# Kernel optimization log

Measured on AMD Instinct MI355X. Metric: run time of the kernel, lower is better.

Reference implementation:

```python
import jax, jax.numpy as jnp
import numpy as np
from jax import lax

NUM_CLASSES = 21      # VOC: background (class 0) + 20 fg classes
TOP_K = 200           # max detections kept per (image, class)
CONF_THRESH = 0.01
NMS_THRESH = 0.45
VAR0, VAR1 = 0.1, 0.2 # cfg.VARIANCE
K_PRE = 256           # candidates pre-selected per class before NMS (fixed-shape NMS)


def setup_inputs() -> dict:
    key = jax.random.key(0)
    k1, k2, k3 = jax.random.split(key, 3)
    B, P, C = 32, 8732, NUM_CLASSES
    loc_data = jax.random.normal(k1, (B, P, 4), dtype=jnp.float32)
    conf_data = jax.random.normal(k2, (B, P, C), dtype=jnp.float32)
    u = jax.random.uniform(k3, (P, 4), dtype=jnp.float32)
    # priors in center-offset form: centers in [0,1), w/h in [0.02, 0.32)
    prior_data = jnp.concatenate([u[:, :2], 0.02 + 0.3 * u[:, 2:]], axis=-1)
    return {"loc_data": loc_data, "conf_data": conf_data, "prior_data": prior_data}


def decode(loc, priors):
    # loc, priors: [..., 4]; priors are (cx, cy, w, h)
    centers = priors[..., :2] + loc[..., :2] * VAR0 * priors[..., 2:]
    wh = priors[..., 2:] * jnp.exp(loc[..., 2:] * VAR1)
    xy_min = centers - wh * 0.5
    return jnp.concatenate([xy_min, xy_min + wh], axis=-1)  # (x1,y1,x2,y2)


def pairwise_iou(b):
    # b: [K, 4] corner boxes -> [K, K] IoU
    area = jnp.maximum(b[:, 2] - b[:, 0], 0.0) * jnp.maximum(b[:, 3] - b[:, 1], 0.0)
    lt = jnp.maximum(b[:, None, :2], b[None, :, :2])
    rb = jnp.minimum(b[:, None, 2:], b[None, :, 2:])
    wh = jnp.clip(rb - lt, 0.0)
    inter = wh[..., 0] * wh[..., 1]
    union = area[:, None] + area[None, :] - inter
    return inter / jnp.maximum(union, 1e-9)


def nms_one_class(scores_p, boxes_p4):
    # scores_p: [P], boxes_p4: [P, 4]; fixed-shape NMS -> [TOP_K, 5] (score, x1, y1, x2, y2)
    vals, idx = lax.top_k(scores_p, K_PRE)          # sorted descending
    cand = boxes_p4[idx]                            # [K_PRE, 4]
    valid = vals > CONF_THRESH
    iou = pairwise_iou(cand)                        # [K_PRE, K_PRE]
    ar = jnp.arange(K_PRE)

    def step(keep, i):
        # a kept box suppresses later boxes overlapping it above threshold
        sup = keep[i] & (iou[i] > NMS_THRESH) & (ar > i)
        return keep & (~sup), None

    keep, _ = lax.scan(step, valid, ar)
    kept_scores = jnp.where(keep, vals, 0.0)
    # kept entries are already score-ordered; pull the top TOP_K survivors to the front
    sv, si = lax.top_k(kept_scores, TOP_K)
    out_boxes = jnp.where(sv[:, None] > 0.0, cand[si], 0.0)
    return jnp.concatenate([sv[:, None], out_boxes], axis=-1)  # [TOP_K, 5]


def reference(loc_data, conf_data, prior_data):
    # loc_data: [B, P, 4], conf_data: [B, P, C], prior_data: [P, 4]
    probs = jax.nn.softmax(conf_data, axis=-1)                     # [B, P, C]
    probs_fg = jnp.swapaxes(probs[..., 1:], 1, 2)                  # [B, C-1, P] (skip background)
    boxes = decode(loc_data, prior_data[None, :, :])               # [B, P, 4]
    # vmap over classes, then over batch
    per_class = jax.vmap(nms_one_class, in_axes=(0, None))         # ([C-1,P],[P,4]) -> [C-1,TOP_K,5]
    per_image = jax.vmap(per_class, in_axes=(0, 0))
    return per_image(probs_fg, boxes)                              # [B, C-1, TOP_K, 5]
```

## Files before the change

kernel.cpp:

```cpp
#include <hip/hip_runtime.h>
#include <stdint.h>

typedef unsigned long long ull;
typedef float f4v __attribute__((ext_vector_type(4)));

#define NUM_CLASSES 21
#define NFG 20
#define TOPK 200
#define KPRE 256
#define CONF_TH 0.01f
#define NMS_TH 0.45f
#define VAR0 0.1f
#define VAR1 0.2f
#define NV16 18
#define T16_LO 0x3C23u
#define T16_HI 0x3F81u
#define BSLOT(g) ((g) + ((g) >> 6))

__global__ __launch_bounds__(256) void rownorm16_kernel(
    const float* __restrict__ conf, float2* __restrict__ norm,
    ushort* __restrict__ probs16, int B, int P) {
    __shared__ __align__(16) float buf[256 * NUM_CLASSES];
    __shared__ __align__(16) ushort b16[NFG * 256];
    const int t = threadIdx.x;
    const int nch = (P + 255) >> 8;

    const int id = blockIdx.x;
    int b, chk;
    if ((B & 7) == 0) {
        int r = id & 7, m = id >> 3;
        int q = m / nch;
        b = r + (q << 3);
        chk = m - q * nch;
    } else {
        b = id / nch;
        chk = id - b * nch;
    }
    const int p0 = chk << 8;
    const int cnt = min(256, P - p0);
    const float* src = conf + ((size_t)b * P + p0) * NUM_CLASSES;

    if (cnt == 256) {
        const f4v* s4 = (const f4v*)src;
        f4v* b4 = (f4v*)buf;
#pragma unroll
        for (int k = 0; k < 6; ++k) {
            int i = (k << 8) + t;
            if (i < (256 * NUM_CLASSES) / 4) b4[i] = s4[i];
        }
    } else {
        int n = cnt * NUM_CLASSES;
        for (int i = t; i < n; i += 256) buf[i] = src[i];
    }
    __syncthreads();

    if (t < cnt) {
        const float* row = buf + t * NUM_CLASSES;
        float x[NUM_CLASSES];
        float mx = row[0];
        x[0] = mx;
#pragma unroll
        for (int j = 1; j < NUM_CLASSES; ++j) { x[j] = row[j]; mx = fmaxf(mx, x[j]); }
        float s = 0.f;
#pragma unroll
        for (int j = 0; j < NUM_CLASSES; ++j) { x[j] = expf(x[j] - mx); s += x[j]; }
        norm[(size_t)b * P + p0 + t] = make_float2(mx, s);
#pragma unroll
        for (int c = 1; c < NUM_CLASSES; ++c) {
            float v = x[c] / s;
            b16[(c - 1) * 256 + t] = (ushort)(__float_as_uint(v) >> 16);
        }
    }
    __syncthreads();

    if (cnt == 256) {
        const uint* s32 = (const uint*)b16;
#pragma unroll
        for (int k = 0; k < 10; ++k) {
            int e = (k << 8) + t;
            int c = e >> 7;
            int q = e & 127;
            uint* dstu = (uint*)(probs16 + ((size_t)b * NFG + c) * P + p0);
            dstu[q] = s32[(c << 7) + q];
        }
    } else {
        for (int e = t; e < NFG * cnt; e += 256) {
            int c = e / cnt;
            int f = e - c * cnt;
            probs16[((size_t)b * NFG + c) * P + p0 + f] = b16[c * 256 + f];
        }
    }
}

__global__ __launch_bounds__(KPRE) void nms_topk_kernel(
    const float* __restrict__ conf, const float2* __restrict__ norm,
    const ushort* __restrict__ probs16, const float* __restrict__ loc,
    const float* __restrict__ prior, float* __restrict__ out, int B, int P) {

    __shared__ ull arr[2 * KPRE];
    __shared__ ull arr2[2 * KPRE];
    __shared__ int wsum[2][4];
    __shared__ int s_cnt;
    __shared__ float4 sbox[KPRE + (KPRE >> 6)];
    __shared__ float sarea[KPRE + (KPRE >> 6)];
    __shared__ ull smask[KPRE][5];
    __shared__ ull kept_mask[4];

    const int t = threadIdx.x;
    const int lane = t & 63;
    const int wid = t >> 6;
    const ull lmask_lt = (1ULL << lane) - 1ULL;

    const int g = blockIdx.x;
    int b, c;
    if ((B & 7) == 0) {
        int k = g >> 3;
        b = ((k / NFG) << 3) + (g & 7);
        c = k - (k / NFG) * NFG;
    } else {
        b = g / NFG;
        c = g - (g / NFG) * NFG;
    }
    const int pair = b * NFG + c;
    const int nq = P >> 1;

    unsigned int u2[NV16];
    {
        const uint* sp16 = (const uint*)(probs16 + (size_t)pair * P);
#pragma unroll
        for (int i = 0; i < NV16; ++i) {
            int q = (i << 8) + t;
            u2[i] = (q < nq) ? sp16[q] : 0u;
        }
    }

    {
        unsigned int lo = T16_LO, hi = T16_HI;
        while (hi - lo > 1u) {
            unsigned int mid = lo + ((hi - lo) >> 1);
            int cc = 0;
#pragma unroll
            for (int i = 0; i < NV16; ++i) {
                cc += __popcll(__ballot((u2[i] & 0xFFFFu) >= mid));
                cc += __popcll(__ballot((u2[i] >> 16) >= mid));
            }
            if (cc >= KPRE / 4) lo = mid; else hi = mid;
        }
        if (lane == 0) wsum[0][wid] = (int)lo;
    }
    __syncthreads();
    unsigned int T16 = (unsigned int)min(min(wsum[0][0], wsum[0][1]),
                                         min(wsum[0][2], wsum[0][3]));

    int nval;
    for (int attempt = 0;; ++attempt) {
        if (t == 0) s_cnt = 0;
        __syncthreads();
        int wtot = 0;
#pragma unroll
        for (int i = 0; i < NV16; ++i) {
            wtot += __popcll(__ballot((u2[i] & 0xFFFFu) >= T16));
            wtot += __popcll(__ballot((u2[i] >> 16) >= T16));
        }
        int wbase = 0;
        if (lane == 0) wbase = atomicAdd(&s_cnt, wtot);
        wbase = __shfl(wbase, 0);
        int run = wbase;
#pragma unroll
        for (int i = 0; i < NV16; ++i) {
#pragma unroll
            for (int h = 0; h < 2; ++h) {
                unsigned int bits16 = h ? (u2[i] >> 16) : (u2[i] & 0xFFFFu);
                bool pred = (bits16 >= T16);
                ull bal = __ballot(pred);
                if (pred) {
                    int slot = run + __popcll(bal & lmask_lt);
                    if (slot < 2 * KPRE)
                        arr[slot] = (ull)(unsigned int)((((i << 8) + t) << 1) + h);
                }
                run += __popcll(bal);
            }
        }
        __syncthreads();
        if (s_cnt <= 2 * KPRE || attempt == 1) { nval = min(s_cnt, 2 * KPRE); break; }
        unsigned int lo = T16, hi = T16_HI;
        int it = 0;
        while (hi - lo > 1u) {
            unsigned int mid = lo + ((hi - lo) >> 1);
            int cc = 0;
#pragma unroll
            for (int i = 0; i < NV16; ++i) {
                cc += __popcll(__ballot((u2[i] & 0xFFFFu) >= mid));
                cc += __popcll(__ballot((u2[i] >> 16) >= mid));
            }
            if (lane == 0) wsum[it & 1][wid] = cc;
            __syncthreads();
            int totc = wsum[it & 1][0] + wsum[it & 1][1] + wsum[it & 1][2] + wsum[it & 1][3];
            if (totc >= KPRE) lo = mid; else hi = mid;
            ++it;
        }
        T16 = lo;
    }

    for (int e = t; e < 2 * KPRE; e += KPRE)
        if (e >= nval) arr[e] = (ull)0xFFFFFFFFu;
    __syncthreads();

    const float* cb = conf + (size_t)b * P * NUM_CLASSES + (c + 1);
    const float2* nb = norm + (size_t)b * P;
    ull k0, k1;
    {
        unsigned int pa = (unsigned int)arr[t];
        unsigned int pb2 = (unsigned int)arr[t + KPRE];
        const bool va = (pa < (unsigned int)P);
        const bool vb = (pb2 < (unsigned int)P);
        float xa = 0.f, xb = 0.f;
        float2 ma = make_float2(0.f, 1.f), mb = make_float2(0.f, 1.f);
        if (va) { xa = cb[(size_t)pa * NUM_CLASSES]; ma = nb[pa]; }
        if (vb) { xb = cb[(size_t)pb2 * NUM_CLASSES]; mb = nb[pb2]; }
        if (va) {
            float v = expf(xa - ma.x) / ma.y;
            k0 = ((ull)__float_as_uint(v) << 32) | (unsigned int)(~pa);
        } else k0 = 0ULL;
        if (vb) {
            float v = expf(xb - mb.x) / mb.y;
            k1 = ((ull)__float_as_uint(v) << 32) | (unsigned int)(~pb2);
        } else k1 = 0ULL;
    }
    __syncthreads();

    {
        int lstage = 0;
#pragma unroll
        for (int kk = 2; kk <= 2 * KPRE; kk <<= 1) {
#pragma unroll
            for (int j = kk >> 1; j > 0; j >>= 1) {
                if (j == KPRE) {
                    ull mx = (k0 > k1) ? k0 : k1;
                    ull mn = (k0 > k1) ? k1 : k0;
                    k0 = mx; k1 = mn;
                } else if (j >= 64) {
                    ull* A = (lstage & 1) ? arr : arr2;
                    ++lstage;
                    A[t] = k0; A[t + KPRE] = k1;
                    __syncthreads();
                    ull o0 = A[t ^ j];
                    ull o1 = A[(t + KPRE) ^ j];
                    bool amLow = ((t & j) == 0);
                    bool d0 = ((t & kk) == 0);
                    bool d1 = (((t + KPRE) & kk) == 0);
                    k0 = (d0 == amLow) ? ((k0 > o0) ? k0 : o0) : ((k0 > o0) ? o0 : k0);
                    k1 = (d1 == amLow) ? ((k1 > o1) ? k1 : o1) : ((k1 > o1) ? o1 : k1);
                } else {
                    ull o0 = __shfl_xor(k0, j);
                    ull o1 = __shfl_xor(k1, j);
                    bool amLow = ((t & j) == 0);
                    bool d0 = ((t & kk) == 0);
                    bool d1 = (((t + KPRE) & kk) == 0);
                    k0 = (d0 == amLow) ? ((k0 > o0) ? k0 : o0) : ((k0 > o0) ? o0 : k0);
                    k1 = (d1 == amLow) ? ((k1 > o1) ? k1 : o1) : ((k1 > o1) ? o1 : k1);
                }
            }
        }
    }
    const ull key = k0;

    float v = __uint_as_float((unsigned int)(key >> 32));
    int idx = (int)(~(unsigned int)(key & 0xFFFFFFFFu));
    if (idx < 0 || idx >= P) { idx = 0; v = 0.f; }

    const float4 lv = *(const float4*)(loc + ((size_t)b * P + idx) * 4);
    const float4 pv = *(const float4*)(prior + (size_t)idx * 4);
    float cx = pv.x + (lv.x * VAR0) * pv.z;
    float cy = pv.y + (lv.y * VAR0) * pv.w;
    float w = pv.z * expf(lv.z * VAR1);
    float h = pv.w * expf(lv.w * VAR1);
    float x1 = cx - w * 0.5f;
    float y1 = cy - h * 0.5f;
    float x2 = x1 + w;
    float y2 = y1 + h;
    float myarea = fmaxf(x2 - x1, 0.f) * fmaxf(y2 - y1, 0.f);

    sbox[BSLOT(t)] = make_float4(x1, y1, x2, y2);
    sarea[BSLOT(t)] = myarea;
    __syncthreads();

#pragma unroll
    for (int rep = 0; rep < 3; ++rep) {
        int pid = t + (rep << 8);
        if (pid < 640) {
            int r, w2;
            if (pid < 64)       { r = pid;                w2 = 0; }
            else if (pid < 192) { int q = pid - 64;  r = 64  + (q >> 1); w2 = q & 1; }
            else if (pid < 384) { int q = pid - 192; int q3 = q / 3; r = 128 + q3; w2 = q - 3 * q3; }
            else                { int q = pid - 384; r = 192 + (q >> 2); w2 = q & 3; }
            float4 rb = sbox[BSLOT(r)];
            float ra = sarea[BSLOT(r)];
            ull mm = 0ULL;
            for (int i = 0; i < 64; ++i) {
                int gg = (w2 << 6) + i;
                float4 gb = sbox[BSLOT(gg)];
                float lx = fmaxf(gb.x, rb.x), ly = fmaxf(gb.y, rb.y);
                float rx = fminf(gb.z, rb.z), ry = fminf(gb.w, rb.w);
                float iw = fmaxf(rx - lx, 0.f), ih = fmaxf(ry - ly, 0.f);
                float inter = iw * ih;
                float uni = sarea[BSLOT(gg)] + ra - inter;
                bool s = (inter / fmaxf(uni, 1e-9f)) > NMS_TH;
                mm |= ((ull)(s ? 1u : 0u)) << i;
            }
            smask[r][w2] = mm;
        }
    }
    __syncthreads();

    ull m0 = smask[t][0];
    ull m1 = (wid >= 1) ? smask[t][1] : 0ULL;
    ull m2 = (wid >= 2) ? smask[t][2] : 0ULL;
    ull m3 = (wid >= 3) ? smask[t][3] : 0ULL;
    if (wid == 0) m0 &= lmask_lt;
    else if (wid == 1) m1 &= lmask_lt;
    else if (wid == 2) m2 &= lmask_lt;
    else m3 &= lmask_lt;

    int alive = (v > CONF_TH) ? 1 : 0;
    ull mykept = 0ULL;
#pragma unroll
    for (int w2 = 0; w2 < 4; ++w2) {
        if (wid == w2) {
            if (w2 > 0 && (m0 & kept_mask[0])) alive = 0;
            if (w2 > 1 && (m1 & kept_mask[1])) alive = 0;
            if (w2 > 2 && (m2 & kept_mask[2])) alive = 0;
            ull mw = (w2 == 0) ? m0 : (w2 == 1) ? m1 : (w2 == 2) ? m2 : m3;
            ull validb = __ballot(alive != 0);
            ull todo = __ballot((mw & validb) != 0ULL) & validb;
            ull kept = validb & ~todo;
            while (todo) {
                int i = __builtin_ctzll(todo);
                ull row = __shfl(mw, i);
                if ((row & kept) == 0ULL) kept |= (1ULL << i);
                todo &= (todo - 1ULL);
            }
            mykept = kept;
            alive = (int)((kept >> lane) & 1ULL);
            if (lane == 0) kept_mask[w2] = kept;
        }
        __syncthreads();
    }

    int rank = 0;
#pragma unroll
    for (int w2 = 0; w2 < 4; ++w2)
        if (w2 < wid) rank += __popcll(kept_mask[w2]);
    rank += __popcll(mykept & lmask_lt);
    int total = 0;
#pragma unroll
    for (int w2 = 0; w2 < 4; ++w2) total += __popcll(kept_mask[w2]);

    float* orow = out + (size_t)pair * TOPK * 5;
    if (alive && rank < TOPK) {
        float* o = orow + rank * 5;
        o[0] = v; o[1] = x1; o[2] = y1; o[3] = x2; o[4] = y2;
    }
    if (t < TOPK && t >= total) {
        float* o = orow + t * 5;
        o[0] = 0.f; o[1] = 0.f; o[2] = 0.f; o[3] = 0.f; o[4] = 0.f;
    }
}

extern "C" void kernel_launch(void* const* d_in, const int* in_sizes, int n_in,
                              void* d_out, int out_size, void* d_ws, size_t ws_size,
                              hipStream_t stream) {
    const float* loc = (const float*)d_in[0];
    const float* conf = (const float*)d_in[1];
    const float* prior = (const float*)d_in[2];
    float* out = (float*)d_out;

    int P = in_sizes[2] / 4;
    int B = in_sizes[0] / (4 * P);
    int nch = (P + 255) / 256;

    float2* norm = (float2*)d_ws;
    ushort* probs16 = (ushort*)((char*)d_ws + (size_t)B * P * 8);

    rownorm16_kernel<<<dim3(B * nch), 256, 0, stream>>>(conf, norm, probs16, B, P);
    nms_topk_kernel<<<B * NFG, KPRE, 0, stream>>>(conf, norm, probs16, loc, prior, out, B, P);
}
```

Baseline: 126.8 us.

## Double NMS block to 512 threads, one sort key per thread

Raises the NMS/top-k kernel block size from 256 to 512 threads. Each thread now holds half as many packed fp16 probabilities for the threshold search and one bitonic sort key instead of two. The IoU mask build needs two passes instead of three. The threshold search, compaction and bitonic sort are restructured to match, which cuts per-thread serial work and register pressure but adds more barriers across 8 waves. Threads 256 and up sit idle during the decode and greedy-suppression phases.

```diff
diff --git a/kernel.cpp b/kernel.cpp
--- a/kernel.cpp
+++ b/kernel.cpp
@@ -8,11 +8,12 @@
 #define NFG 20
 #define TOPK 200
 #define KPRE 256
+#define NTHR 512
 #define CONF_TH 0.01f
 #define NMS_TH 0.45f
 #define VAR0 0.1f
 #define VAR1 0.2f
-#define NV16 18
+#define NV9 9
 #define T16_LO 0x3C23u
 #define T16_HI 0x3F81u
 #define BSLOT(g) ((g) + ((g) >> 6))
@@ -92,14 +93,14 @@
     }
 }
 
-__global__ __launch_bounds__(KPRE) void nms_topk_kernel(
+__global__ __launch_bounds__(NTHR) void nms_topk_kernel(
     const float* __restrict__ conf, const float2* __restrict__ norm,
     const ushort* __restrict__ probs16, const float* __restrict__ loc,
     const float* __restrict__ prior, float* __restrict__ out, int B, int P) {
 
     __shared__ ull arr[2 * KPRE];
     __shared__ ull arr2[2 * KPRE];
-    __shared__ int wsum[2][4];
+    __shared__ int wsum[2][8];
     __shared__ int s_cnt;
     __shared__ float4 sbox[KPRE + (KPRE >> 6)];
     __shared__ float sarea[KPRE + (KPRE >> 6)];
@@ -124,12 +125,12 @@
     const int pair = b * NFG + c;
     const int nq = P >> 1;
 
-    unsigned int u2[NV16];
+    unsigned int u2[NV9];
     {
         const uint* sp16 = (const uint*)(probs16 + (size_t)pair * P);
 #pragma unroll
-        for (int i = 0; i < NV16; ++i) {
-            int q = (i << 8) + t;
+        for (int i = 0; i < NV9; ++i) {
+            int q = (i << 9) + t;
             u2[i] = (q < nq) ? sp16[q] : 0u;
         }
     }
@@ -140,17 +141,22 @@
             unsigned int mid = lo + ((hi - lo) >> 1);
             int cc = 0;
 #pragma unroll
-            for (int i = 0; i < NV16; ++i) {
+            for (int i = 0; i < NV9; ++i) {
                 cc += __popcll(__ballot((u2[i] & 0xFFFFu) >= mid));
                 cc += __popcll(__ballot((u2[i] >> 16) >= mid));
             }
-            if (cc >= KPRE / 4) lo = mid; else hi = mid;
+            if (cc >= KPRE / 8) lo = mid; else hi = mid;
         }
         if (lane == 0) wsum[0][wid] = (int)lo;
     }
     __syncthreads();
-    unsigned int T16 = (unsigned int)min(min(wsum[0][0], wsum[0][1]),
-                                         min(wsum[0][2], wsum[0][3]));
+    unsigned int T16;
+    {
+        int m = wsum[0][0];
+#pragma unroll
+        for (int w = 1; w < 8; ++w) m = min(m, wsum[0][w]);
+        T16 = (unsigned int)m;
+    }
 
     int nval;
     for (int attempt = 0;; ++attempt) {
@@ -158,7 +164,7 @@
         __syncthreads();
         int wtot = 0;
 #pragma unroll
-        for (int i = 0; i < NV16; ++i) {
+        for (int i = 0; i < NV9; ++i) {
             wtot += __popcll(__ballot((u2[i] & 0xFFFFu) >= T16));
             wtot += __popcll(__ballot((u2[i] >> 16) >= T16));
         }
@@ -167,7 +173,7 @@
         wbase = __shfl(wbase, 0);
         int run = wbase;
 #pragma unroll
-        for (int i = 0; i < NV16; ++i) {
+        for (int i = 0; i < NV9; ++i) {
 #pragma unroll
             for (int h = 0; h < 2; ++h) {
                 unsigned int bits16 = h ? (u2[i] >> 16) : (u2[i] & 0xFFFFu);
@@ -176,7 +182,7 @@
                 if (pred) {
                     int slot = run + __popcll(bal & lmask_lt);
                     if (slot < 2 * KPRE)
-                        arr[slot] = (ull)(unsigned int)((((i << 8) + t) << 1) + h);
+                        arr[slot] = (ull)(unsigned int)((((i << 9) + t) << 1) + h);
                 }
                 run += __popcll(bal);
             }
@@ -189,43 +195,37 @@
             unsigned int mid = lo + ((hi - lo) >> 1);
             int cc = 0;
 #pragma unroll
-            for (int i = 0; i < NV16; ++i) {
+            for (int i = 0; i < NV9; ++i) {
                 cc += __popcll(__ballot((u2[i] & 0xFFFFu) >= mid));
                 cc += __popcll(__ballot((u2[i] >> 16) >= mid));
             }
             if (lane == 0) wsum[it & 1][wid] = cc;
             __syncthreads();
-            int totc = wsum[it & 1][0] + wsum[it & 1][1] + wsum[it & 1][2] + wsum[it & 1][3];
+            int totc = 0;
+#pragma unroll
+            for (int w = 0; w < 8; ++w) totc += wsum[it & 1][w];
             if (totc >= KPRE) lo = mid; else hi = mid;
             ++it;
         }
         T16 = lo;
     }
 
-    for (int e = t; e < 2 * KPRE; e += KPRE)
-        if (e >= nval) arr[e] = (ull)0xFFFFFFFFu;
+    if (t >= nval) arr[t] = (ull)0xFFFFFFFFu;
     __syncthreads();
 
     const float* cb = conf + (size_t)b * P * NUM_CLASSES + (c + 1);
     const float2* nb = norm + (size_t)b * P;
-    ull k0, k1;
+    ull k0;
     {
         unsigned int pa = (unsigned int)arr[t];
-        unsigned int pb2 = (unsigned int)arr[t + KPRE];
-        const bool va = (pa < (unsigned int)P);
-        const bool vb = (pb2 < (unsigned int)P);
-        float xa = 0.f, xb = 0.f;
-        float2 ma = make_float2(0.f, 1.f), mb = make_float2(0.f, 1.f);
-        if (va) { xa = cb[(size_t)pa * NUM_CLASSES]; ma = nb[pa]; }
-        if (vb) { xb = cb[(size_t)pb2 * NUM_CLASSES]; mb = nb[pb2]; }
-        if (va) {
+        if (pa < (unsigned int)P) {
+            float xa = cb[(size_t)pa * NUM_CLASSES];
+            float2 ma = nb[pa];
             float v = expf(xa - ma.x) / ma.y;
             k0 = ((ull)__float_as_uint(v) << 32) | (unsigned int)(~pa);
-        } else k0 = 0ULL;
-        if (vb) {
-            float v = expf(xb - mb.x) / mb.y;
-            k1 = ((ull)__float_as_uint(v) << 32) | (unsigned int)(~pb2);
-        } else k1 = 0ULL;
+        } else {
+            k0 = 0ULL;
+        }
     }
     __syncthreads();
 
@@ -235,59 +235,49 @@
         for (int kk = 2; kk <= 2 * KPRE; kk <<= 1) {
 #pragma unroll
             for (int j = kk >> 1; j > 0; j >>= 1) {
-                if (j == KPRE) {
-                    ull mx = (k0 > k1) ? k0 : k1;
-                    ull mn = (k0 > k1) ? k1 : k0;
-                    k0 = mx; k1 = mn;
-                } else if (j >= 64) {
+                bool amLow = ((t & j) == 0);
+                bool d0 = ((t & kk) == 0);
+                if (j >= 64) {
                     ull* A = (lstage & 1) ? arr : arr2;
                     ++lstage;
-                    A[t] = k0; A[t + KPRE] = k1;
+                    A[t] = k0;
                     __syncthreads();
                     ull o0 = A[t ^ j];
-                    ull o1 = A[(t + KPRE) ^ j];
-                    bool amLow = ((t & j) == 0);
-                    bool d0 = ((t & kk) == 0);
-                    bool d1 = (((t + KPRE) & kk) == 0);
                     k0 = (d0 == amLow) ? ((k0 > o0) ? k0 : o0) : ((k0 > o0) ? o0 : k0);
-                    k1 = (d1 == amLow) ? ((k1 > o1) ? k1 : o1) : ((k1 > o1) ? o1 : k1);
                 } else {
                     ull o0 = __shfl_xor(k0, j);
-                    ull o1 = __shfl_xor(k1, j);
-                    bool amLow = ((t & j) == 0);
-                    bool d0 = ((t & kk) == 0);
-                    bool d1 = (((t + KPRE) & kk) == 0);
                     k0 = (d0 == amLow) ? ((k0 > o0) ? k0 : o0) : ((k0 > o0) ? o0 : k0);
-                    k1 = (d1 == amLow) ? ((k1 > o1) ? k1 : o1) : ((k1 > o1) ? o1 : k1);
                 }
             }
         }
     }
     const ull key = k0;
 
-    float v = __uint_as_float((unsigned int)(key >> 32));
-    int idx = (int)(~(unsigned int)(key & 0xFFFFFFFFu));
-    if (idx < 0 || idx >= P) { idx = 0; v = 0.f; }
-
-    const float4 lv = *(const float4*)(loc + ((size_t)b * P + idx) * 4);
-    const float4 pv = *(const float4*)(prior + (size_t)idx * 4);
-    float cx = pv.x + (lv.x * VAR0) * pv.z;
-    float cy = pv.y + (lv.y * VAR0) * pv.w;
-    float w = pv.z * expf(lv.z * VAR1);
-    float h = pv.w * expf(lv.w * VAR1);
-    float x1 = cx - w * 0.5f;
-    float y1 = cy - h * 0.5f;
-    float x2 = x1 + w;
-    float y2 = y1 + h;
-    float myarea = fmaxf(x2 - x1, 0.f) * fmaxf(y2 - y1, 0.f);
-
-    sbox[BSLOT(t)] = make_float4(x1, y1, x2, y2);
-    sarea[BSLOT(t)] = myarea;
-    __syncthreads();
-
-#pragma unroll
-    for (int rep = 0; rep < 3; ++rep) {
-        int pid = t + (rep << 8);
+    float v = 0.f, x1 = 0.f, y1 = 0.f, x2 = 0.f, y2 = 0.f;
+    if (t < KPRE) {
+        v = __uint_as_float((unsigned int)(key >> 32));
+        int idx = (int)(~(unsigned int)(key & 0xFFFFFFFFu));
+        if (idx < 0 || idx >= P) { idx = 0; v = 0.f; }
+
+        const float4 lv = *(const float4*)(loc + ((size_t)b * P + idx) * 4);
+        const float4 pv = *(const float4*)(prior + (size_t)idx * 4);
+        float cx = pv.x + (lv.x * VAR0) * pv.z;
+        float cy = pv.y + (lv.y * VAR0) * pv.w;
+        float w = pv.z * expf(lv.z * VAR1);
+        float h = pv.w * expf(lv.w * VAR1);
+        x1 = cx - w * 0.5f;
+        y1 = cy - h * 0.5f;
+        x2 = x1 + w;
+        y2 = y1 + h;
+        float myarea = fmaxf(x2 - x1, 0.f) * fmaxf(y2 - y1, 0.f);
+        sbox[BSLOT(t)] = make_float4(x1, y1, x2, y2);
+        sarea[BSLOT(t)] = myarea;
+    }
+    __syncthreads();
+
+#pragma unroll
+    for (int rep = 0; rep < 2; ++rep) {
+        int pid = t + (rep << 9);
         if (pid < 640) {
             int r, w2;
             if (pid < 64)       { r = pid;                w2 = 0; }
@@ -313,16 +303,19 @@
     }
     __syncthreads();
 
-    ull m0 = smask[t][0];
-    ull m1 = (wid >= 1) ? smask[t][1] : 0ULL;
-    ull m2 = (wid >= 2) ? smask[t][2] : 0ULL;
-    ull m3 = (wid >= 3) ? smask[t][3] : 0ULL;
-    if (wid == 0) m0 &= lmask_lt;
-    else if (wid == 1) m1 &= lmask_lt;
-    else if (wid == 2) m2 &= lmask_lt;
-    else m3 &= lmask_lt;
-
-    int alive = (v > CONF_TH) ? 1 : 0;
+    ull m0 = 0ULL, m1 = 0ULL, m2 = 0ULL, m3 = 0ULL;
+    if (t < KPRE) {
+        m0 = smask[t][0];
+        m1 = (wid >= 1) ? smask[t][1] : 0ULL;
+        m2 = (wid >= 2) ? smask[t][2] : 0ULL;
+        m3 = (wid >= 3) ? smask[t][3] : 0ULL;
+        if (wid == 0) m0 &= lmask_lt;
+        else if (wid == 1) m1 &= lmask_lt;
+        else if (wid == 2) m2 &= lmask_lt;
+        else m3 &= lmask_lt;
+    }
+
+    int alive = (t < KPRE && v > CONF_TH) ? 1 : 0;
     ull mykept = 0ULL;
 #pragma unroll
     for (int w2 = 0; w2 < 4; ++w2) {
@@ -383,5 +376,5 @@
     ushort* probs16 = (ushort*)((char*)d_ws + (size_t)B * P * 8);
 
     rownorm16_kernel<<<dim3(B * nch), 256, 0, stream>>>(conf, norm, probs16, B, P);
-    nms_topk_kernel<<<B * NFG, KPRE, 0, stream>>>(conf, norm, probs16, loc, prior, out, B, P);
+    nms_topk_kernel<<<B * NFG, NTHR, 0, stream>>>(conf, norm, probs16, loc, prior, out, B, P);
 }
```

Result: faster. 123.0 us (-3.0%).
